# Optimization experiments

Measured on AMD Instinct MI355X. Metric: run time of the kernel, lower is better.

Reference implementation:

```python
import jax, jax.numpy as jnp
import numpy as np
import math

T, B, N, D = 4, 4, 1024, 512
H = 8
HD = D // H
EPS = 1e-6


def setup_inputs() -> dict:
    key = jax.random.key(0)
    ks = jax.random.split(key, 9)
    s = 1.0 / math.sqrt(D)
    inp = {"x": jax.random.normal(ks[0], (T, B, N, D), dtype=jnp.float32)}
    names = ["wq", "wk", "wv", "wo"]
    for i, nm in enumerate(names):
        inp[nm] = jax.random.uniform(ks[1 + i], (D, D), dtype=jnp.float32, minval=-s, maxval=s)
        inp["b" + nm[1]] = jax.random.uniform(ks[5 + i], (D,), dtype=jnp.float32, minval=-s, maxval=s)
    return inp


def reference(x, wq, bq, wk, bk, wv, bv, wo, bo):
    t, b, n, d = x.shape
    # torch Linear: y = x @ W.T + bias
    q = x @ wq.T + bq
    k = x @ wk.T + bk
    v = x @ wv.T + bv
    # (t, b, n, H, HD) -> (t, b, H, n, HD)
    qh = q.reshape(t, b, n, H, HD).transpose(0, 1, 3, 2, 4)
    kh = k.reshape(t, b, n, H, HD).transpose(0, 1, 3, 2, 4)
    vh = v.reshape(t, b, n, H, HD).transpose(0, 1, 3, 2, 4)
    scores = jnp.einsum("tbhqd,tbhkd->tbhqk", qh, kh) / math.sqrt(HD)
    attn = jax.nn.relu(scores)
    attn = attn / (attn.sum(axis=-1, keepdims=True) + EPS)
    ctx = jnp.einsum("tbhqk,tbhkd->tbhqd", attn, vh)
    out = ctx.transpose(0, 1, 3, 2, 4).reshape(t, b, n, d)
    return out @ wo.T + bo
```

## Files before the change

### kernel.cpp

```cpp
#include <hip/hip_runtime.h>

typedef unsigned short u16;
typedef __attribute__((ext_vector_type(8))) short bf16x8;
typedef __attribute__((ext_vector_type(4))) float f32x4;
typedef __attribute__((ext_vector_type(16))) float f32x16;
typedef __attribute__((ext_vector_type(2))) unsigned int u32x2;

__device__ inline u16 f2b(float f) {
    unsigned u;
    __builtin_memcpy(&u, &f, 4);
    unsigned r = u + 0x7FFF + ((u >> 16) & 1);
    return (u16)(r >> 16);
}

__device__ inline bf16x8 pack8(const float* p) {
    union { u16 us[8]; bf16x8 v; } r;
#pragma unroll
    for (int i = 0; i < 8; i++) r.us[i] = f2b(p[i]);
    return r.v;
}

__device__ inline unsigned cvtpk(float lo, float hi) {
    unsigned r;
    asm("v_cvt_pk_bf16_f32 %0, %1, %2" : "=v"(r) : "v"(lo), "v"(hi));
    return r;
}

__device__ inline void gload16(const void* g, void* l) {
    __builtin_amdgcn_global_load_lds((__attribute__((address_space(1))) void*)g,
                                     (__attribute__((address_space(3))) void*)l, 16, 0, 0);
}

__global__ __launch_bounds__(256) void conv_kernel(const float* __restrict__ x,
                                                   const float* __restrict__ wq,
                                                   const float* __restrict__ wk,
                                                   const float* __restrict__ wv,
                                                   const float* __restrict__ wo,
                                                   u16* __restrict__ xb, u16* __restrict__ wb) {
    const int bid = blockIdx.x;
    const float* src;
    u16* dst;
    size_t base;
    if (bid < 4096) {
        src = x; dst = xb; base = (size_t)bid * 2048;
    } else {
        const int wsel = (bid - 4096) >> 7;
        src = (wsel == 0) ? wq : (wsel == 1) ? wk : (wsel == 2) ? wv : wo;
        dst = wb + (size_t)wsel * 262144;
        base = (size_t)((bid - 4096) & 127) * 2048;
    }
    const size_t idx = base + (size_t)threadIdx.x * 8;
    float a[8];
    *(float4*)&a[0] = *(const float4*)&src[idx];
    *(float4*)&a[4] = *(const float4*)&src[idx + 4];
    *(bf16x8*)&dst[idx] = pack8(a);
}

template <int MODE>
__global__ __launch_bounds__(256) void gemm_kernel(const u16* __restrict__ A,
                                                   const u16* __restrict__ W,
                                                   const float* __restrict__ B0,
                                                   const float* __restrict__ B1,
                                                   const float* __restrict__ B2,
                                                   void* __restrict__ O0v, u16* __restrict__ O1,
                                                   u16* __restrict__ O2) {
    const int m0 = blockIdx.x * 128;
    const int n0 = blockIdx.y * 128;
    const int seg = (MODE == 0) ? (n0 >> 9) : 0;
    const int nl0 = (MODE == 0) ? (n0 & 511) : n0;
    const float* Bb = (seg == 0) ? B0 : (seg == 1) ? B1 : B2;
    u16* O = (seg == 0) ? (u16*)O0v : (seg == 1) ? O1 : O2;

    __shared__ __align__(16) u16 Al[2][128 * 32];
    __shared__ __align__(16) u16 Bl[2][128 * 32];

    const int tid = threadIdx.x;
    const int lane = tid & 63, wave = tid >> 6;
    const int quad = lane >> 4, col = lane & 15;
    const int wm = wave >> 1, wn = wave & 1;

    int srow[2], ssc[2];
#pragma unroll
    for (int i = 0; i < 2; i++) {
        const int cl = tid + i * 256;
        srow[i] = cl >> 2;
        ssc[i] = (((cl & 3) ^ ((srow[i] >> 1) & 3))) * 8;
    }
    const int cswz = quad ^ ((col >> 1) & 3);

#define GSTAGE(BUF, K0)                                                                   \
    {                                                                                     \
        _Pragma("unroll") for (int i_ = 0; i_ < 2; i_++) {                                \
            const int cl_ = tid + i_ * 256;                                               \
            gload16(&A[(size_t)(m0 + srow[i_]) * 512 + (K0) + ssc[i_]], &Al[BUF][cl_ * 8]); \
        }                                                                                 \
        _Pragma("unroll") for (int i_ = 0; i_ < 2; i_++) {                                \
            const int cl_ = tid + i_ * 256;                                               \
            gload16(&W[(size_t)(n0 + srow[i_]) * 512 + (K0) + ssc[i_]], &Bl[BUF][cl_ * 8]); \
        }                                                                                 \
    }

    f32x4 acc[4][4];
#pragma unroll
    for (int i = 0; i < 4; i++)
#pragma unroll
        for (int j = 0; j < 4; j++) acc[i][j] = (f32x4){0.f, 0.f, 0.f, 0.f};

    GSTAGE(0, 0)
    __syncthreads();

    int bufi = 0;
    for (int k0 = 0; k0 < 512; k0 += 32) {
        if (k0 < 480) GSTAGE(bufi ^ 1, k0 + 32)

        bf16x8 af[4], bfr[4];
#pragma unroll
        for (int t = 0; t < 4; t++) {
            af[t] = *(const bf16x8*)&Al[bufi][((wm * 64 + t * 16 + col) * 4 + cswz) * 8];
            bfr[t] = *(const bf16x8*)&Bl[bufi][((wn * 64 + t * 16 + col) * 4 + cswz) * 8];
        }
        __builtin_amdgcn_s_setprio(1);
#pragma unroll
        for (int i = 0; i < 4; i++)
#pragma unroll
            for (int j = 0; j < 4; j++)
                acc[i][j] = __builtin_amdgcn_mfma_f32_16x16x32_bf16(af[i], bfr[j], acc[i][j], 0, 0, 0);
        __builtin_amdgcn_s_setprio(0);
        __syncthreads();
        bufi ^= 1;
    }
#undef GSTAGE

    float bias[4];
#pragma unroll
    for (int j = 0; j < 4; j++) bias[j] = Bb[nl0 + wn * 64 + j * 16 + col];

#pragma unroll
    for (int i = 0; i < 4; i++) {
        const int mbase = m0 + wm * 64 + i * 16 + quad * 4;
#pragma unroll
        for (int j = 0; j < 4; j++) {
            const int nl = nl0 + wn * 64 + j * 16 + col;
            if (MODE == 1) {
                float* Of = (float*)O0v;
#pragma unroll
                for (int r = 0; r < 4; r++)
                    Of[(size_t)(mbase + r) * 512 + nl] = acc[i][j][r] + bias[j];
            } else {
                const int h = nl >> 6, hd = nl & 63;
                if (seg < 2) {
                    const float qs = (seg == 0) ? 0.125f : 1.f;
#pragma unroll
                    for (int r = 0; r < 4; r++) {
                        int m = mbase + r;
                        int s = m >> 10, tok = m & 1023;
                        O[(size_t)((s * 8 + h) * 1024 + tok) * 64 + hd] =
                            f2b((acc[i][j][r] + bias[j]) * qs);
                    }
                } else {
                    int s = mbase >> 10, tok0 = mbase & 1023;
                    union { u16 us[4]; uint2 v; } pk;
#pragma unroll
                    for (int r = 0; r < 4; r++) pk.us[r] = f2b(acc[i][j][r] + bias[j]);
                    *(uint2*)&O[(size_t)((s * 8 + h) * 64 + hd) * 1024 + tok0] = pk.v;
                }
            }
        }
    }
}

__global__ __launch_bounds__(256, 2) void attn_kernel(const u16* __restrict__ Q,
                                                      const u16* __restrict__ Kp,
                                                      const u16* __restrict__ Vt,
                                                      u16* __restrict__ Ctx) {
    __shared__ __align__(16) u16 Kl[2][4096];
    __shared__ __align__(16) u16 Vl[2][4096];

    const int bid = blockIdx.x;
    const int head = bid & 127;
    const int qt = bid >> 7;
    const int s = head >> 3, h = head & 7;
    const u16* Qh = Q + (size_t)head * 65536;
    const u16* Kh = Kp + (size_t)head * 65536;
    const u16* Vh = Vt + (size_t)head * 65536;

    const int tid = threadIdx.x;
    const int lane = tid & 63, wave = tid >> 6;
    const int l31 = lane & 31, hi = lane >> 5;
    const int q0 = qt * 256 + wave * 64;
    const int cx = l31 & 7;

    int srow[2], sxc[2];
#pragma unroll
    for (int i = 0; i < 2; i++) {
        const int p = tid + i * 256;
        srow[i] = p >> 3;
        sxc[i] = (p & 7) ^ (srow[i] & 7);
    }

#define STAGE(B, K0)                                                                    \
    {                                                                                   \
        _Pragma("unroll") for (int i_ = 0; i_ < 2; i_++) {                              \
            const int p_ = tid + i_ * 256;                                              \
            gload16(&Kh[(size_t)((K0) + srow[i_]) * 64 + sxc[i_] * 8], &Kl[B][p_ * 8]); \
        }                                                                               \
        _Pragma("unroll") for (int i_ = 0; i_ < 2; i_++) {                              \
            const int p_ = tid + i_ * 256;                                              \
            gload16(&Vh[(size_t)srow[i_] * 1024 + (K0) + sxc[i_] * 8], &Vl[B][p_ * 8]); \
        }                                                                               \
    }

    union { u16 us[8]; bf16x8 v; } one;
#pragma unroll
    for (int i = 0; i < 8; i++) one.us[i] = 0x3F80;
    const bf16x8 onesf = one.v;

    bf16x8 qf[2][4];
#pragma unroll
    for (int q2 = 0; q2 < 2; q2++)
#pragma unroll
        for (int kk = 0; kk < 4; kk++)
            qf[q2][kk] =
                *(const bf16x8*)&Qh[(size_t)(q0 + q2 * 32 + l31) * 64 + kk * 16 + hi * 8];

    f32x16 cacc[2][2];
    f32x16 dacc[2];
#pragma unroll
    for (int q2 = 0; q2 < 2; q2++) {
#pragma unroll
        for (int r = 0; r < 16; r++) {
            cacc[q2][0][r] = 0.f;
            cacc[q2][1][r] = 0.f;
            dacc[q2][r] = 0.f;
        }
    }

    STAGE(0, 0)
    __syncthreads();

    int buf = 0;
    for (int kt = 0; kt < 16; kt++) {
        if (kt < 15) STAGE(buf ^ 1, (kt + 1) * 64)

        bf16x8 pa[2][4];
#pragma unroll
        for (int mt = 0; mt < 2; mt++) {
            f32x16 s0, s1;
#pragma unroll
            for (int r = 0; r < 16; r++) { s0[r] = 0.f; s1[r] = 0.f; }
            __builtin_amdgcn_s_setprio(1);
#pragma unroll
            for (int kk = 0; kk < 4; kk++) {
                const bf16x8 kf =
                    *(const bf16x8*)&Kl[buf][((mt * 32 + l31) * 8 + ((2 * kk + hi) ^ cx)) * 8];
                s0 = __builtin_amdgcn_mfma_f32_32x32x16_bf16(kf, qf[0][kk], s0, 0, 0, 0);
                s1 = __builtin_amdgcn_mfma_f32_32x32x16_bf16(kf, qf[1][kk], s1, 0, 0, 0);
            }
            __builtin_amdgcn_s_setprio(0);

#pragma unroll
            for (int q2 = 0; q2 < 2; q2++) {
                const f32x16& sc = q2 ? s1 : s0;
                const unsigned c0 = cvtpk(fmaxf(sc[0], 0.f), fmaxf(sc[1], 0.f));
                const unsigned c1 = cvtpk(fmaxf(sc[2], 0.f), fmaxf(sc[3], 0.f));
                const unsigned c2 = cvtpk(fmaxf(sc[4], 0.f), fmaxf(sc[5], 0.f));
                const unsigned c3 = cvtpk(fmaxf(sc[6], 0.f), fmaxf(sc[7], 0.f));
                const unsigned c4 = cvtpk(fmaxf(sc[8], 0.f), fmaxf(sc[9], 0.f));
                const unsigned c5 = cvtpk(fmaxf(sc[10], 0.f), fmaxf(sc[11], 0.f));
                const unsigned c6 = cvtpk(fmaxf(sc[12], 0.f), fmaxf(sc[13], 0.f));
                const unsigned c7 = cvtpk(fmaxf(sc[14], 0.f), fmaxf(sc[15], 0.f));
                const u32x2 s02 = __builtin_amdgcn_permlane32_swap(c0, c2, false, false);
                const u32x2 s13 = __builtin_amdgcn_permlane32_swap(c1, c3, false, false);
                const u32x2 s46 = __builtin_amdgcn_permlane32_swap(c4, c6, false, false);
                const u32x2 s57 = __builtin_amdgcn_permlane32_swap(c5, c7, false, false);
                union { unsigned u[4]; bf16x8 v; } f0u, f1u;
                f0u.u[0] = s02.x; f0u.u[1] = s13.x; f0u.u[2] = s02.y; f0u.u[3] = s13.y;
                f1u.u[0] = s46.x; f1u.u[1] = s57.x; f1u.u[2] = s46.y; f1u.u[3] = s57.y;
                pa[q2][mt * 2 + 0] = f0u.v;
                pa[q2][mt * 2 + 1] = f1u.v;
            }
        }

        __builtin_amdgcn_s_setprio(1);
#pragma unroll
        for (int kg = 0; kg < 4; kg++) {
            const bf16x8 vf0 = *(const bf16x8*)&Vl[buf][(l31 * 8 + ((2 * kg + hi) ^ cx)) * 8];
            const bf16x8 vf1 =
                *(const bf16x8*)&Vl[buf][((32 + l31) * 8 + ((2 * kg + hi) ^ cx)) * 8];
            dacc[0] = __builtin_amdgcn_mfma_f32_32x32x16_bf16(pa[0][kg], onesf, dacc[0], 0, 0, 0);
            dacc[1] = __builtin_amdgcn_mfma_f32_32x32x16_bf16(pa[1][kg], onesf, dacc[1], 0, 0, 0);
            cacc[0][0] = __builtin_amdgcn_mfma_f32_32x32x16_bf16(pa[0][kg], vf0, cacc[0][0], 0, 0, 0);
            cacc[0][1] = __builtin_amdgcn_mfma_f32_32x32x16_bf16(pa[0][kg], vf1, cacc[0][1], 0, 0, 0);
            cacc[1][0] = __builtin_amdgcn_mfma_f32_32x32x16_bf16(pa[1][kg], vf0, cacc[1][0], 0, 0, 0);
            cacc[1][1] = __builtin_amdgcn_mfma_f32_32x32x16_bf16(pa[1][kg], vf1, cacc[1][1], 0, 0, 0);
        }
        __builtin_amdgcn_s_setprio(0);

        __syncthreads();
        buf ^= 1;
    }
#undef STAGE

#pragma unroll
    for (int q2 = 0; q2 < 2; q2++) {
#pragma unroll
        for (int r = 0; r < 16; r++) {
            const int ql = (r & 3) + 8 * (r >> 2) + 4 * hi;
            const float inv = 1.f / (dacc[q2][r] + 1e-6f);
            const size_t grow = (size_t)(s * 1024 + q0 + q2 * 32 + ql);
            Ctx[grow * 512 + h * 64 + l31] = f2b(cacc[q2][0][r] * inv);
            Ctx[grow * 512 + h * 64 + 32 + l31] = f2b(cacc[q2][1][r] * inv);
        }
    }
}

extern "C" void kernel_launch(void* const* d_in, const int* in_sizes, int n_in, void* d_out,
                              int out_size, void* d_ws, size_t ws_size, hipStream_t stream) {
    const float* x = (const float*)d_in[0];
    const float* wq = (const float*)d_in[1];
    const float* bq = (const float*)d_in[2];
    const float* wk = (const float*)d_in[3];
    const float* bk = (const float*)d_in[4];
    const float* wv = (const float*)d_in[5];
    const float* bv = (const float*)d_in[6];
    const float* wo = (const float*)d_in[7];
    const float* bo = (const float*)d_in[8];

    const size_t E = 16384ull * 512ull;
    u16* xb = (u16*)d_ws;
    u16* cw = xb;
    u16* wb = xb + E;
    u16* qw = wb + 4 * 262144;
    u16* kw = qw + E;
    u16* vw = kw + E;

    conv_kernel<<<dim3(4096 + 512), 256, 0, stream>>>(x, wq, wk, wv, wo, xb, wb);
    gemm_kernel<0><<<dim3(128, 12), 256, 0, stream>>>(xb, wb, bq, bk, bv, qw, kw, vw);
    attn_kernel<<<dim3(512), 256, 0, stream>>>(qw, kw, vw, cw);
    gemm_kernel<1><<<dim3(128, 4), 256, 0, stream>>>(cw, wb + 3 * 262144, bo, nullptr, nullptr,
                                                     d_out, nullptr, nullptr);
}
```

Baseline: 191.0 us.

## Double K/V tile depth to 128 keys and interleave PV MFMAs per subtile

```diff
diff --git a/kernel.cpp b/kernel.cpp
--- a/kernel.cpp
+++ b/kernel.cpp
@@ -173,8 +173,8 @@
                                                       const u16* __restrict__ Kp,
                                                       const u16* __restrict__ Vt,
                                                       u16* __restrict__ Ctx) {
-    __shared__ __align__(16) u16 Kl[2][4096];
-    __shared__ __align__(16) u16 Vl[2][4096];
+    __shared__ __align__(16) u16 Kl[2][8192];
+    __shared__ __align__(16) u16 Vl[2][8192];
 
     const int bid = blockIdx.x;
     const int head = bid & 127;
@@ -190,24 +190,26 @@
     const int q0 = qt * 256 + wave * 64;
     const int cx = l31 & 7;
 
-    int srow[2], sxc[2];
-#pragma unroll
-    for (int i = 0; i < 2; i++) {
+    int offK[4], offV[4];
+#pragma unroll
+    for (int i = 0; i < 4; i++) {
         const int p = tid + i * 256;
-        srow[i] = p >> 3;
-        sxc[i] = (p & 7) ^ (srow[i] & 7);
-    }
-
-#define STAGE(B, K0)                                                                    \
-    {                                                                                   \
-        _Pragma("unroll") for (int i_ = 0; i_ < 2; i_++) {                              \
-            const int p_ = tid + i_ * 256;                                              \
-            gload16(&Kh[(size_t)((K0) + srow[i_]) * 64 + sxc[i_] * 8], &Kl[B][p_ * 8]); \
-        }                                                                               \
-        _Pragma("unroll") for (int i_ = 0; i_ < 2; i_++) {                              \
-            const int p_ = tid + i_ * 256;                                              \
-            gload16(&Vh[(size_t)srow[i_] * 1024 + (K0) + sxc[i_] * 8], &Vl[B][p_ * 8]); \
-        }                                                                               \
+        const int kr = p >> 3, kc = (p & 7) ^ (kr & 7);
+        offK[i] = kr * 64 + kc * 8;
+        const int vr = p >> 4, vc = (p & 15) ^ (vr & 7);
+        offV[i] = vr * 1024 + vc * 8;
+    }
+
+#define STAGE(B, K0)                                                            \
+    {                                                                           \
+        _Pragma("unroll") for (int i_ = 0; i_ < 4; i_++) {                      \
+            const int p_ = tid + i_ * 256;                                      \
+            gload16(&Kh[(size_t)(K0) * 64 + offK[i_]], &Kl[B][p_ * 8]);         \
+        }                                                                       \
+        _Pragma("unroll") for (int i_ = 0; i_ < 4; i_++) {                      \
+            const int p_ = tid + i_ * 256;                                      \
+            gload16(&Vh[(size_t)(K0) + offV[i_]], &Vl[B][p_ * 8]);              \
+        }                                                                       \
     }
 
     union { u16 us[8]; bf16x8 v; } one;
@@ -239,12 +241,11 @@
     __syncthreads();
 
     int buf = 0;
-    for (int kt = 0; kt < 16; kt++) {
-        if (kt < 15) STAGE(buf ^ 1, (kt + 1) * 64)
-
-        bf16x8 pa[2][4];
-#pragma unroll
-        for (int mt = 0; mt < 2; mt++) {
+    for (int kt = 0; kt < 8; kt++) {
+        if (kt < 7) STAGE(buf ^ 1, (kt + 1) * 128)
+
+#pragma unroll
+        for (int mt = 0; mt < 4; mt++) {
             f32x16 s0, s1;
 #pragma unroll
             for (int r = 0; r < 16; r++) { s0[r] = 0.f; s1[r] = 0.f; }
@@ -258,6 +259,7 @@
             }
             __builtin_amdgcn_s_setprio(0);
 
+            bf16x8 paq[2][2];
 #pragma unroll
             for (int q2 = 0; q2 < 2; q2++) {
                 const f32x16& sc = q2 ? s1 : s0;
@@ -276,25 +278,32 @@
                 union { unsigned u[4]; bf16x8 v; } f0u, f1u;
                 f0u.u[0] = s02.x; f0u.u[1] = s13.x; f0u.u[2] = s02.y; f0u.u[3] = s13.y;
                 f1u.u[0] = s46.x; f1u.u[1] = s57.x; f1u.u[2] = s46.y; f1u.u[3] = s57.y;
-                pa[q2][mt * 2 + 0] = f0u.v;
-                pa[q2][mt * 2 + 1] = f1u.v;
+                paq[q2][0] = f0u.v;
+                paq[q2][1] = f1u.v;
             }
-        }
-
-        __builtin_amdgcn_s_setprio(1);
-#pragma unroll
-        for (int kg = 0; kg < 4; kg++) {
-            const bf16x8 vf0 = *(const bf16x8*)&Vl[buf][(l31 * 8 + ((2 * kg + hi) ^ cx)) * 8];
-            const bf16x8 vf1 =
-                *(const bf16x8*)&Vl[buf][((32 + l31) * 8 + ((2 * kg + hi) ^ cx)) * 8];
-            dacc[0] = __builtin_amdgcn_mfma_f32_32x32x16_bf16(pa[0][kg], onesf, dacc[0], 0, 0, 0);
-            dacc[1] = __builtin_amdgcn_mfma_f32_32x32x16_bf16(pa[1][kg], onesf, dacc[1], 0, 0, 0);
-            cacc[0][0] = __builtin_amdgcn_mfma_f32_32x32x16_bf16(pa[0][kg], vf0, cacc[0][0], 0, 0, 0);
-            cacc[0][1] = __builtin_amdgcn_mfma_f32_32x32x16_bf16(pa[0][kg], vf1, cacc[0][1], 0, 0, 0);
-            cacc[1][0] = __builtin_amdgcn_mfma_f32_32x32x16_bf16(pa[1][kg], vf0, cacc[1][0], 0, 0, 0);
-            cacc[1][1] = __builtin_amdgcn_mfma_f32_32x32x16_bf16(pa[1][kg], vf1, cacc[1][1], 0, 0, 0);
-        }
-        __builtin_amdgcn_s_setprio(0);
+
+            const bf16x8 vfa0 = *(const bf16x8*)&Vl[buf][(l31 * 16 + ((4 * mt + hi) ^ cx)) * 8];
+            const bf16x8 vfa1 =
+                *(const bf16x8*)&Vl[buf][((32 + l31) * 16 + ((4 * mt + hi) ^ cx)) * 8];
+            const bf16x8 vfb0 =
+                *(const bf16x8*)&Vl[buf][(l31 * 16 + ((4 * mt + 2 + hi) ^ cx)) * 8];
+            const bf16x8 vfb1 =
+                *(const bf16x8*)&Vl[buf][((32 + l31) * 16 + ((4 * mt + 2 + hi) ^ cx)) * 8];
+            __builtin_amdgcn_s_setprio(1);
+            dacc[0] = __builtin_amdgcn_mfma_f32_32x32x16_bf16(paq[0][0], onesf, dacc[0], 0, 0, 0);
+            cacc[0][0] = __builtin_amdgcn_mfma_f32_32x32x16_bf16(paq[0][0], vfa0, cacc[0][0], 0, 0, 0);
+            cacc[0][1] = __builtin_amdgcn_mfma_f32_32x32x16_bf16(paq[0][0], vfa1, cacc[0][1], 0, 0, 0);
+            dacc[1] = __builtin_amdgcn_mfma_f32_32x32x16_bf16(paq[1][0], onesf, dacc[1], 0, 0, 0);
+            cacc[1][0] = __builtin_amdgcn_mfma_f32_32x32x16_bf16(paq[1][0], vfa0, cacc[1][0], 0, 0, 0);
+            cacc[1][1] = __builtin_amdgcn_mfma_f32_32x32x16_bf16(paq[1][0], vfa1, cacc[1][1], 0, 0, 0);
+            dacc[0] = __builtin_amdgcn_mfma_f32_32x32x16_bf16(paq[0][1], onesf, dacc[0], 0, 0, 0);
+            cacc[0][0] = __builtin_amdgcn_mfma_f32_32x32x16_bf16(paq[0][1], vfb0, cacc[0][0], 0, 0, 0);
+            cacc[0][1] = __builtin_amdgcn_mfma_f32_32x32x16_bf16(paq[0][1], vfb1, cacc[0][1], 0, 0, 0);
+            dacc[1] = __builtin_amdgcn_mfma_f32_32x32x16_bf16(paq[1][1], onesf, dacc[1], 0, 0, 0);
+            cacc[1][0] = __builtin_amdgcn_mfma_f32_32x32x16_bf16(paq[1][1], vfb0, cacc[1][0], 0, 0, 0);
+            cacc[1][1] = __builtin_amdgcn_mfma_f32_32x32x16_bf16(paq[1][1], vfb1, cacc[1][1], 0, 0, 0);
+            __builtin_amdgcn_s_setprio(0);
+        }
 
         __syncthreads();
         buf ^= 1;
```

After: 189.1 us. Within noise of the previous version (-1.0%).
